# Kernel optimization log

Measured on AMD Instinct MI355X. Metric: run time of the kernel, lower is better.

Reference implementation:

```python
import jax, jax.numpy as jnp
import numpy as np

B, S, H = 32, 4096, 512


def setup_inputs() -> dict:
    key = jax.random.key(0)
    ks = jax.random.split(key, 8)
    scale = 1.0 / np.sqrt(H)
    return {
        "query": jax.random.normal(ks[0], (B, H), dtype=jnp.float32),
        "keys": jax.random.normal(ks[1], (B, S, 2 * H), dtype=jnp.float32),
        "Wa_w": jax.random.uniform(ks[2], (H, H), jnp.float32, -scale, scale),
        "Wa_b": jax.random.uniform(ks[3], (H,), jnp.float32, -scale, scale),
        "Ua_w": jax.random.uniform(ks[4], (H, 2 * H), jnp.float32, -scale, scale),
        "Ua_b": jax.random.uniform(ks[5], (H,), jnp.float32, -scale, scale),
        "Va_w": jax.random.uniform(ks[6], (1, H), jnp.float32, -scale, scale),
        "Va_b": jax.random.uniform(ks[7], (1,), jnp.float32, -scale, scale),
    }


def reference(query, keys, Wa_w, Wa_b, Ua_w, Ua_b, Va_w, Va_b):
    # query: [B,H], keys: [B,S,2H]
    q_proj = query @ Wa_w.T + Wa_b                       # [B,H]
    k_proj = jnp.einsum('bsk,hk->bsh', keys, Ua_w) + Ua_b  # [B,S,H]
    energy = jnp.tanh(q_proj[:, None, :] + k_proj)        # [B,S,H]
    scores = jnp.einsum('bsh,h->bs', energy, Va_w[0]) + Va_b[0]  # [B,S]
    attn_weights = jax.nn.softmax(scores, axis=1)         # [B,S]
    context = jnp.einsum('bs,bsk->bk', attn_weights, keys)  # [B,2H]
    return (context, attn_weights)
```

## Files before the change

kernel.cpp:

```cpp
#include <hip/hip_runtime.h>
#include <hip/hip_bf16.h>
#include <cstdint>
#include <cstddef>

#define NB 32
#define NS 4096
#define NH 512
#define NK 1024

typedef __attribute__((ext_vector_type(8))) short bf16x8;
typedef __attribute__((ext_vector_type(4))) float f32x4;

__device__ __forceinline__ short f2bf_s(float f) {
  union { float f; unsigned u; } x; x.f = f;
  unsigned r = x.u + 0x7fffu + ((x.u >> 16) & 1u);
  return (short)(r >> 16);
}

__global__ void k_ua_cvt(const float* __restrict__ ua, unsigned short* __restrict__ out) {
  int i = (blockIdx.x * 256 + threadIdx.x) * 4;
  float4 v = *(const float4*)(ua + i);
  ushort4 o;
  o.x = (unsigned short)f2bf_s(v.x);
  o.y = (unsigned short)f2bf_s(v.y);
  o.z = (unsigned short)f2bf_s(v.z);
  o.w = (unsigned short)f2bf_s(v.w);
  *(ushort4*)(out + i) = o;
}

__global__ void k_qproj(const float* __restrict__ q, const float* __restrict__ ww,
                        const float* __restrict__ wb, const float* __restrict__ ub,
                        float* __restrict__ qp) {
  int b = blockIdx.y;
  int h = blockIdx.x * 128 + threadIdx.x;
  const float* qr = q + b * NH;
  const float* wr = ww + h * NH;
  float acc = 0.f;
  for (int k = 0; k < NH; k += 4) {
    float4 a = *(const float4*)(qr + k);
    float4 c = *(const float4*)(wr + k);
    acc += a.x * c.x + a.y * c.y + a.z * c.z + a.w * c.w;
  }
  qp[b * NH + h] = acc + wb[h] + ub[h];
}

__global__ __launch_bounds__(512, 2)
void k_scores(const float* __restrict__ keys, const unsigned short* __restrict__ uabf,
              const float* __restrict__ qproj, const float* __restrict__ vaw,
              const float* __restrict__ vab, float* __restrict__ scores) {
  __shared__ uint4 lds4[2560];
  __shared__ float va_s[512];
  __shared__ float qp_s[512];

  const int b   = blockIdx.y;
  const int s0  = blockIdx.x * 128;
  const int tid = threadIdx.x;
  const int w   = tid >> 6;
  const int l   = tid & 63;
  const int col = l & 15;
  const int g   = l >> 4;

  va_s[tid] = vaw[tid];
  qp_s[tid] = qproj[b * NH + tid];

  f32x4 zero = {0.f, 0.f, 0.f, 0.f};
  f32x4 acc[32];
  #pragma unroll
  for (int i = 0; i < 32; ++i) acc[i] = zero;

  const float* arow = keys + ((size_t)b * NS + (size_t)(s0 + w * 16 + col)) * NK;

  for (int ks = 0; ks < 32; ++ks) {
    const int k0 = ks * 32;
    __syncthreads();
    #pragma unroll
    for (int i = 0; i < 4; ++i) {
      int c = (i << 9) | tid;
      int n = c >> 2, kc = c & 3;
      uint4 v = *(const uint4*)(uabf + (n << 10) + k0 + (kc << 3));
      lds4[n * 5 + kc] = v;
    }
    __syncthreads();

    const float* ap = arow + k0 + g * 8;
    float4 a0 = *(const float4*)(ap);
    float4 a1 = *(const float4*)(ap + 4);
    bf16x8 af;
    af[0] = f2bf_s(a0.x); af[1] = f2bf_s(a0.y); af[2] = f2bf_s(a0.z); af[3] = f2bf_s(a0.w);
    af[4] = f2bf_s(a1.x); af[5] = f2bf_s(a1.y); af[6] = f2bf_s(a1.z); af[7] = f2bf_s(a1.w);

    #pragma unroll
    for (int nt = 0; nt < 32; ++nt) {
      int n = (nt << 4) | col;
      bf16x8 bf = *(const bf16x8*)&lds4[n * 5 + g];
      acc[nt] = __builtin_amdgcn_mfma_f32_16x16x32_bf16(af, bf, acc[nt], 0, 0, 0);
    }
  }

  #pragma unroll
  for (int j = 0; j < 4; ++j) {
    float sc = 0.f;
    #pragma unroll
    for (int nt = 0; nt < 32; ++nt) {
      int n = (nt << 4) | col;
      sc += va_s[n] * tanhf(qp_s[n] + acc[nt][j]);
    }
    sc += __shfl_xor(sc, 1);
    sc += __shfl_xor(sc, 2);
    sc += __shfl_xor(sc, 4);
    sc += __shfl_xor(sc, 8);
    if (col == 0)
      scores[(size_t)b * NS + s0 + w * 16 + g * 4 + j] = sc + vab[0];
  }
}

__global__ void k_softmax(const float* __restrict__ scores, float* __restrict__ attn) {
  __shared__ float redm[4];
  __shared__ float reds[4];
  int b = blockIdx.x, tid = threadIdx.x;
  const float* row = scores + (size_t)b * NS;
  float v[16];
  float m = -1e30f;
  #pragma unroll
  for (int i = 0; i < 16; ++i) { v[i] = row[i * 256 + tid]; m = fmaxf(m, v[i]); }
  #pragma unroll
  for (int off = 1; off < 64; off <<= 1) m = fmaxf(m, __shfl_xor(m, off));
  if ((tid & 63) == 0) redm[tid >> 6] = m;
  __syncthreads();
  m = fmaxf(fmaxf(redm[0], redm[1]), fmaxf(redm[2], redm[3]));
  float s = 0.f;
  #pragma unroll
  for (int i = 0; i < 16; ++i) { v[i] = expf(v[i] - m); s += v[i]; }
  #pragma unroll
  for (int off = 1; off < 64; off <<= 1) s += __shfl_xor(s, off);
  if ((tid & 63) == 0) reds[tid >> 6] = s;
  __syncthreads();
  s = reds[0] + reds[1] + reds[2] + reds[3];
  float inv = 1.f / s;
  float* o = attn + (size_t)b * NS;
  #pragma unroll
  for (int i = 0; i < 16; ++i) o[i * 256 + tid] = v[i] * inv;
}

__global__ void k_ctx_partial(const float* __restrict__ keys, const float* __restrict__ attn,
                              float* __restrict__ part) {
  __shared__ float w_s[256];
  int b = blockIdx.y, seg = blockIdx.x, tid = threadIdx.x;
  int sbeg = seg * 256;
  w_s[tid] = attn[(size_t)b * NS + sbeg + tid];
  __syncthreads();
  const float* kp = keys + ((size_t)b * NS + sbeg) * NK + tid * 4;
  float ax = 0.f, ay = 0.f, az = 0.f, aw = 0.f;
  #pragma unroll 4
  for (int s = 0; s < 256; ++s) {
    float4 kv = *(const float4*)(kp + (size_t)s * NK);
    float wv = w_s[s];
    ax += wv * kv.x; ay += wv * kv.y; az += wv * kv.z; aw += wv * kv.w;
  }
  float4 o; o.x = ax; o.y = ay; o.z = az; o.w = aw;
  *(float4*)(part + ((size_t)(seg * NB + b) << 10) + tid * 4) = o;
}

__global__ void k_ctx_reduce(const float* __restrict__ part, float* __restrict__ ctx) {
  int i = blockIdx.x * 256 + threadIdx.x;
  int b = i >> 10, c = i & 1023;
  float s = 0.f;
  #pragma unroll
  for (int seg = 0; seg < 16; ++seg) s += part[((size_t)(seg * NB + b) << 10) + c];
  ctx[i] = s;
}

extern "C" void kernel_launch(void* const* d_in, const int* in_sizes, int n_in,
                              void* d_out, int out_size, void* d_ws, size_t ws_size,
                              hipStream_t stream) {
  const float* query = (const float*)d_in[0];
  const float* keys  = (const float*)d_in[1];
  const float* Wa_w  = (const float*)d_in[2];
  const float* Wa_b  = (const float*)d_in[3];
  const float* Ua_w  = (const float*)d_in[4];
  const float* Ua_b  = (const float*)d_in[5];
  const float* Va_w  = (const float*)d_in[6];
  const float* Va_b  = (const float*)d_in[7];

  float* out      = (float*)d_out;
  float* ctx_out  = out;
  float* attn_out = out + NB * NK;

  unsigned short* ua_bf = (unsigned short*)d_ws;
  float* qproj  = (float*)((char*)d_ws + (1u << 20));
  float* scores = (float*)((char*)d_ws + (1u << 20) + (1u << 16));
  float* part   = (float*)((char*)d_ws + (1u << 20) + (1u << 16) + (1u << 19));

  k_ua_cvt<<<512, 256, 0, stream>>>(Ua_w, ua_bf);
  k_qproj<<<dim3(4, NB), 128, 0, stream>>>(query, Wa_w, Wa_b, Ua_b, qproj);
  k_scores<<<dim3(NS / 128, NB), 512, 0, stream>>>(keys, ua_bf, qproj, Va_w, Va_b, scores);
  k_softmax<<<NB, 256, 0, stream>>>(scores, attn_out);
  k_ctx_partial<<<dim3(16, NB), 256, 0, stream>>>(keys, attn_out, part);
  k_ctx_reduce<<<NB * NK / 256, 256, 0, stream>>>(part, ctx_out);
}
```

Measured before the change: 472.8 us.

## Restructure scores GEMM with 32x32 MFMA, LDS-staged keys and prepacked Ua weights

Rewrites the scores kernel. Keys tiles are converted to bf16 and staged into double-buffered, XOR-swizzled LDS with prefetch of the next chunk, and Ua is prepacked into an MFMA-fragment layout read directly from global memory. Each wave now computes a 64x128 tile with 32x32x16 MFMAs instead of 16x16x32, which gives more reuse per fragment load. Also swaps tanhf for an exp-based fast tanh and adds a cross-wave LDS reduction. The cost is higher register pressure from the 8 accumulator tiles, plus a small precision change in tanh.

```diff
diff --git a/kernel.cpp b/kernel.cpp
--- a/kernel.cpp
+++ b/kernel.cpp
@@ -7,25 +7,31 @@
 #define NS 4096
 #define NH 512
 #define NK 1024
+#define KC 64
 
 typedef __attribute__((ext_vector_type(8))) short bf16x8;
 typedef __attribute__((ext_vector_type(4))) float f32x4;
-
-__device__ __forceinline__ short f2bf_s(float f) {
+typedef __attribute__((ext_vector_type(16))) float f32x16;
+
+__device__ __forceinline__ unsigned short f2bf_s(float f) {
   union { float f; unsigned u; } x; x.f = f;
   unsigned r = x.u + 0x7fffu + ((x.u >> 16) & 1u);
-  return (short)(r >> 16);
-}
-
-__global__ void k_ua_cvt(const float* __restrict__ ua, unsigned short* __restrict__ out) {
-  int i = (blockIdx.x * 256 + threadIdx.x) * 4;
-  float4 v = *(const float4*)(ua + i);
-  ushort4 o;
-  o.x = (unsigned short)f2bf_s(v.x);
-  o.y = (unsigned short)f2bf_s(v.y);
-  o.z = (unsigned short)f2bf_s(v.z);
-  o.w = (unsigned short)f2bf_s(v.w);
-  *(ushort4*)(out + i) = o;
+  return (unsigned short)(r >> 16);
+}
+
+__global__ void k_ua_pack(const float* __restrict__ ua, unsigned short* __restrict__ out) {
+  int t = blockIdx.x * 256 + threadIdx.x;
+  int l = t & 63;
+  int ct = (t >> 6) & 15;
+  int kk = t >> 10;
+  const float* src = ua + (size_t)(ct * 32 + (l & 31)) * NK + kk * 16 + (l >> 5) * 8;
+  float4 a = *(const float4*)src;
+  float4 c = *(const float4*)(src + 4);
+  ushort4 o0, o1;
+  o0.x = f2bf_s(a.x); o0.y = f2bf_s(a.y); o0.z = f2bf_s(a.z); o0.w = f2bf_s(a.w);
+  o1.x = f2bf_s(c.x); o1.y = f2bf_s(c.y); o1.z = f2bf_s(c.z); o1.w = f2bf_s(c.w);
+  ushort4* dst = (ushort4*)(out + (size_t)t * 8);
+  dst[0] = o0; dst[1] = o1;
 }
 
 __global__ void k_qproj(const float* __restrict__ q, const float* __restrict__ ww,
@@ -45,72 +51,139 @@
 }
 
 __global__ __launch_bounds__(512, 2)
-void k_scores(const float* __restrict__ keys, const unsigned short* __restrict__ uabf,
-              const float* __restrict__ qproj, const float* __restrict__ vaw,
-              const float* __restrict__ vab, float* __restrict__ scores) {
-  __shared__ uint4 lds4[2560];
-  __shared__ float va_s[512];
-  __shared__ float qp_s[512];
+void k_scores2(const float* __restrict__ keys, const unsigned short* __restrict__ uapk,
+               const float* __restrict__ qproj, const float* __restrict__ vaw,
+               const float* __restrict__ vab, float* __restrict__ scores) {
+  __shared__ alignas(16) unsigned short A_lds[2][128 * KC];
+  __shared__ float qp_s[NH];
+  __shared__ float va_s[NH];
+  __shared__ float red[128][4];
 
   const int b   = blockIdx.y;
   const int s0  = blockIdx.x * 128;
   const int tid = threadIdx.x;
   const int w   = tid >> 6;
   const int l   = tid & 63;
-  const int col = l & 15;
-  const int g   = l >> 4;
-
+  const int rg  = w >> 2;
+  const int cg  = w & 3;
+  const int l31 = l & 31;
+  const int lhi = l >> 5;
+
+  qp_s[tid] = qproj[b * NH + tid];
   va_s[tid] = vaw[tid];
-  qp_s[tid] = qproj[b * NH + tid];
-
-  f32x4 zero = {0.f, 0.f, 0.f, 0.f};
-  f32x4 acc[32];
-  #pragma unroll
-  for (int i = 0; i < 32; ++i) acc[i] = zero;
-
-  const float* arow = keys + ((size_t)b * NS + (size_t)(s0 + w * 16 + col)) * NK;
-
-  for (int ks = 0; ks < 32; ++ks) {
-    const int k0 = ks * 32;
-    __syncthreads();
+
+  const int sr  = tid & 127;
+  const int skq = tid >> 7;
+  const float* kbase = keys + ((size_t)b * NS + s0 + sr) * NK + skq * 16;
+  char* const myrow = (char*)&A_lds[0][0];
+  const int wr0 = sr * 128;
+  const int wo0 = (skq * 32) ^ ((sr & 7) << 4);
+  const int wo1 = (skq * 32 + 16) ^ ((sr & 7) << 4);
+
+  f32x16 acc[2][4];
+  #pragma unroll
+  for (int i = 0; i < 2; ++i)
     #pragma unroll
-    for (int i = 0; i < 4; ++i) {
-      int c = (i << 9) | tid;
-      int n = c >> 2, kc = c & 3;
-      uint4 v = *(const uint4*)(uabf + (n << 10) + k0 + (kc << 3));
-      lds4[n * 5 + kc] = v;
-    }
-    __syncthreads();
-
-    const float* ap = arow + k0 + g * 8;
-    float4 a0 = *(const float4*)(ap);
-    float4 a1 = *(const float4*)(ap + 4);
-    bf16x8 af;
-    af[0] = f2bf_s(a0.x); af[1] = f2bf_s(a0.y); af[2] = f2bf_s(a0.z); af[3] = f2bf_s(a0.w);
-    af[4] = f2bf_s(a1.x); af[5] = f2bf_s(a1.y); af[6] = f2bf_s(a1.z); af[7] = f2bf_s(a1.w);
-
+    for (int j = 0; j < 4; ++j)
+      #pragma unroll
+      for (int e = 0; e < 16; ++e) acc[i][j][e] = 0.f;
+
+  const int arow0 = rg * 64 + 0 * 32 + l31;
+  const int arow1 = rg * 64 + 1 * 32 + l31;
+  const int asw0 = (arow0 & 7) << 4;
+  const int asw1 = (arow1 & 7) << 4;
+
+  {
+    float4 st0 = *(const float4*)(kbase + 0);
+    float4 st1 = *(const float4*)(kbase + 4);
+    float4 st2 = *(const float4*)(kbase + 8);
+    float4 st3 = *(const float4*)(kbase + 12);
+    ushort4 p0, p1, p2, p3;
+    p0.x=f2bf_s(st0.x); p0.y=f2bf_s(st0.y); p0.z=f2bf_s(st0.z); p0.w=f2bf_s(st0.w);
+    p1.x=f2bf_s(st1.x); p1.y=f2bf_s(st1.y); p1.z=f2bf_s(st1.z); p1.w=f2bf_s(st1.w);
+    p2.x=f2bf_s(st2.x); p2.y=f2bf_s(st2.y); p2.z=f2bf_s(st2.z); p2.w=f2bf_s(st2.w);
+    p3.x=f2bf_s(st3.x); p3.y=f2bf_s(st3.y); p3.z=f2bf_s(st3.z); p3.w=f2bf_s(st3.w);
+    *(ushort4*)(myrow + wr0 + wo0)     = p0;
+    *(ushort4*)(myrow + wr0 + wo0 + 8) = p1;
+    *(ushort4*)(myrow + wr0 + wo1)     = p2;
+    *(ushort4*)(myrow + wr0 + wo1 + 8) = p3;
+  }
+  __syncthreads();
+
+  for (int c = 0; c < 16; ++c) {
+    const int buf = c & 1;
+    const char* Ab = (const char*)&A_lds[buf][0];
+    float4 nx0, nx1, nx2, nx3;
+    if (c < 15) {
+      const float* nb = kbase + (c + 1) * KC;
+      nx0 = *(const float4*)(nb + 0);
+      nx1 = *(const float4*)(nb + 4);
+      nx2 = *(const float4*)(nb + 8);
+      nx3 = *(const float4*)(nb + 12);
+    }
     #pragma unroll
-    for (int nt = 0; nt < 32; ++nt) {
-      int n = (nt << 4) | col;
-      bf16x8 bf = *(const bf16x8*)&lds4[n * 5 + g];
-      acc[nt] = __builtin_amdgcn_mfma_f32_16x16x32_bf16(af, bf, acc[nt], 0, 0, 0);
-    }
-  }
-
-  #pragma unroll
-  for (int j = 0; j < 4; ++j) {
-    float sc = 0.f;
+    for (int kk = 0; kk < 4; ++kk) {
+      const int kb = kk * 32 + lhi * 16;
+      bf16x8 af0 = *(const bf16x8*)(Ab + arow0 * 128 + (kb ^ asw0));
+      bf16x8 af1 = *(const bf16x8*)(Ab + arow1 * 128 + (kb ^ asw1));
+      const int kkg = c * 4 + kk;
+      const unsigned short* bp = uapk + (((size_t)kkg * 16 + cg * 4) * 64 + l) * 8;
+      bf16x8 bf0 = *(const bf16x8*)(bp);
+      bf16x8 bf1 = *(const bf16x8*)(bp + 64 * 8);
+      bf16x8 bf2 = *(const bf16x8*)(bp + 128 * 8);
+      bf16x8 bf3 = *(const bf16x8*)(bp + 192 * 8);
+      acc[0][0] = __builtin_amdgcn_mfma_f32_32x32x16_bf16(af0, bf0, acc[0][0], 0, 0, 0);
+      acc[1][0] = __builtin_amdgcn_mfma_f32_32x32x16_bf16(af1, bf0, acc[1][0], 0, 0, 0);
+      acc[0][1] = __builtin_amdgcn_mfma_f32_32x32x16_bf16(af0, bf1, acc[0][1], 0, 0, 0);
+      acc[1][1] = __builtin_amdgcn_mfma_f32_32x32x16_bf16(af1, bf1, acc[1][1], 0, 0, 0);
+      acc[0][2] = __builtin_amdgcn_mfma_f32_32x32x16_bf16(af0, bf2, acc[0][2], 0, 0, 0);
+      acc[1][2] = __builtin_amdgcn_mfma_f32_32x32x16_bf16(af1, bf2, acc[1][2], 0, 0, 0);
+      acc[0][3] = __builtin_amdgcn_mfma_f32_32x32x16_bf16(af0, bf3, acc[0][3], 0, 0, 0);
+      acc[1][3] = __builtin_amdgcn_mfma_f32_32x32x16_bf16(af1, bf3, acc[1][3], 0, 0, 0);
+    }
+    if (c < 15) {
+      char* Aw = (char*)&A_lds[buf ^ 1][0];
+      ushort4 p0, p1, p2, p3;
+      p0.x=f2bf_s(nx0.x); p0.y=f2bf_s(nx0.y); p0.z=f2bf_s(nx0.z); p0.w=f2bf_s(nx0.w);
+      p1.x=f2bf_s(nx1.x); p1.y=f2bf_s(nx1.y); p1.z=f2bf_s(nx1.z); p1.w=f2bf_s(nx1.w);
+      p2.x=f2bf_s(nx2.x); p2.y=f2bf_s(nx2.y); p2.z=f2bf_s(nx2.z); p2.w=f2bf_s(nx2.w);
+      p3.x=f2bf_s(nx3.x); p3.y=f2bf_s(nx3.y); p3.z=f2bf_s(nx3.z); p3.w=f2bf_s(nx3.w);
+      *(ushort4*)(Aw + wr0 + wo0)     = p0;
+      *(ushort4*)(Aw + wr0 + wo0 + 8) = p1;
+      *(ushort4*)(Aw + wr0 + wo1)     = p2;
+      *(ushort4*)(Aw + wr0 + wo1 + 8) = p3;
+      __syncthreads();
+    }
+  }
+
+  #pragma unroll
+  for (int rt = 0; rt < 2; ++rt) {
     #pragma unroll
-    for (int nt = 0; nt < 32; ++nt) {
-      int n = (nt << 4) | col;
-      sc += va_s[n] * tanhf(qp_s[n] + acc[nt][j]);
-    }
-    sc += __shfl_xor(sc, 1);
-    sc += __shfl_xor(sc, 2);
-    sc += __shfl_xor(sc, 4);
-    sc += __shfl_xor(sc, 8);
-    if (col == 0)
-      scores[(size_t)b * NS + s0 + w * 16 + g * 4 + j] = sc + vab[0];
+    for (int reg = 0; reg < 16; ++reg) {
+      float sum = 0.f;
+      #pragma unroll
+      for (int ct = 0; ct < 4; ++ct) {
+        int n = cg * 128 + ct * 32 + l31;
+        float x = qp_s[n] + acc[rt][ct][reg];
+        float e = __expf(2.f * x);
+        float th = 1.f - 2.f / (e + 1.f);
+        sum += va_s[n] * th;
+      }
+      sum += __shfl_xor(sum, 1);
+      sum += __shfl_xor(sum, 2);
+      sum += __shfl_xor(sum, 4);
+      sum += __shfl_xor(sum, 8);
+      sum += __shfl_xor(sum, 16);
+      if (l31 == 0) {
+        int rloc = (reg & 3) + 8 * (reg >> 2) + 4 * lhi;
+        red[rg * 64 + rt * 32 + rloc][cg] = sum;
+      }
+    }
+  }
+  __syncthreads();
+  if (tid < 128) {
+    float s = red[tid][0] + red[tid][1] + red[tid][2] + red[tid][3] + vab[0];
+    scores[(size_t)b * NS + s0 + tid] = s;
   }
 }
 
@@ -186,14 +259,14 @@
   float* ctx_out  = out;
   float* attn_out = out + NB * NK;
 
-  unsigned short* ua_bf = (unsigned short*)d_ws;
+  unsigned short* ua_pk = (unsigned short*)d_ws;
   float* qproj  = (float*)((char*)d_ws + (1u << 20));
   float* scores = (float*)((char*)d_ws + (1u << 20) + (1u << 16));
   float* part   = (float*)((char*)d_ws + (1u << 20) + (1u << 16) + (1u << 19));
 
-  k_ua_cvt<<<512, 256, 0, stream>>>(Ua_w, ua_bf);
+  k_ua_pack<<<256, 256, 0, stream>>>(Ua_w, ua_pk);
   k_qproj<<<dim3(4, NB), 128, 0, stream>>>(query, Wa_w, Wa_b, Ua_b, qproj);
-  k_scores<<<dim3(NS / 128, NB), 512, 0, stream>>>(keys, ua_bf, qproj, Va_w, Va_b, scores);
+  k_scores2<<<dim3(NS / 128, NB), 512, 0, stream>>>(keys, ua_pk, qproj, Va_w, Va_b, scores);
   k_softmax<<<NB, 256, 0, stream>>>(scores, attn_out);
   k_ctx_partial<<<dim3(16, NB), 256, 0, stream>>>(keys, attn_out, part);
   k_ctx_reduce<<<NB * NK / 256, 256, 0, stream>>>(part, ctx_out);
```

Measured after the change: 577.4 us. 22.1% more time.

## Retile scores GEMM into 256x256 blocks with double-buffered swizzled LDS staging

Applied to the files above, without the earlier changes.

Replaces the scores GEMM with a 256-row by 256-column tiled MFMA kernel. Keys are converted to bf16 into XOR-swizzled LDS, and the pre-packed, swizzled Ua weight is streamed in with direct global-to-LDS loads, both double-buffered across K chunks. Partial scores over two hidden-dimension halves are summed in softmax, tanh is replaced by a fast exp-based form, and the context partial segments are doubled in length. The aim is more reuse per LDS load and overlap of loads with MFMA, at the cost of larger LDS use, extra partial-score traffic and slightly lower tanh accuracy.

```diff
diff --git a/kernel.cpp b/kernel.cpp
--- a/kernel.cpp
+++ b/kernel.cpp
@@ -8,24 +8,36 @@
 #define NH 512
 #define NK 1024
 
-typedef __attribute__((ext_vector_type(8))) short bf16x8;
+typedef __attribute__((ext_vector_type(8))) short short8;
 typedef __attribute__((ext_vector_type(4))) float f32x4;
 
-__device__ __forceinline__ short f2bf_s(float f) {
+__device__ __forceinline__ unsigned short f2bf_s(float f) {
   union { float f; unsigned u; } x; x.f = f;
   unsigned r = x.u + 0x7fffu + ((x.u >> 16) & 1u);
-  return (short)(r >> 16);
-}
-
-__global__ void k_ua_cvt(const float* __restrict__ ua, unsigned short* __restrict__ out) {
-  int i = (blockIdx.x * 256 + threadIdx.x) * 4;
-  float4 v = *(const float4*)(ua + i);
-  ushort4 o;
-  o.x = (unsigned short)f2bf_s(v.x);
-  o.y = (unsigned short)f2bf_s(v.y);
-  o.z = (unsigned short)f2bf_s(v.z);
-  o.w = (unsigned short)f2bf_s(v.w);
-  *(ushort4*)(out + i) = o;
+  return (unsigned short)(r >> 16);
+}
+
+__device__ __forceinline__ void gload16(const void* g, void* l) {
+  __builtin_amdgcn_global_load_lds(
+      (const __attribute__((address_space(1))) unsigned int*)g,
+      (__attribute__((address_space(3))) unsigned int*)l, 16, 0, 0);
+}
+
+__global__ void k_ua_pack(const float* __restrict__ ua, unsigned short* __restrict__ out) {
+  int t = blockIdx.x * 256 + threadIdx.x;
+  int c = t & 2047;
+  int kc = (t >> 11) & 15;
+  int bn = t >> 15;
+  int nloc = c >> 3;
+  int k16 = (c & 7) ^ (nloc & 7);
+  const float* src = ua + (size_t)(bn * 256 + nloc) * NK + kc * 64 + k16 * 8;
+  float4 a = *(const float4*)src;
+  float4 b2 = *(const float4*)(src + 4);
+  ushort4 o0, o1;
+  o0.x = f2bf_s(a.x);  o0.y = f2bf_s(a.y);  o0.z = f2bf_s(a.z);  o0.w = f2bf_s(a.w);
+  o1.x = f2bf_s(b2.x); o1.y = f2bf_s(b2.y); o1.z = f2bf_s(b2.z); o1.w = f2bf_s(b2.w);
+  ushort4* dst = (ushort4*)(out + (size_t)t * 8);
+  dst[0] = o0; dst[1] = o1;
 }
 
 __global__ void k_qproj(const float* __restrict__ q, const float* __restrict__ ww,
@@ -45,84 +57,186 @@
 }
 
 __global__ __launch_bounds__(512, 2)
-void k_scores(const float* __restrict__ keys, const unsigned short* __restrict__ uabf,
-              const float* __restrict__ qproj, const float* __restrict__ vaw,
-              const float* __restrict__ vab, float* __restrict__ scores) {
-  __shared__ uint4 lds4[2560];
-  __shared__ float va_s[512];
-  __shared__ float qp_s[512];
-
-  const int b   = blockIdx.y;
-  const int s0  = blockIdx.x * 128;
-  const int tid = threadIdx.x;
-  const int w   = tid >> 6;
-  const int l   = tid & 63;
-  const int col = l & 15;
-  const int g   = l >> 4;
-
+void k_scores3(const float* __restrict__ keys, const unsigned short* __restrict__ uapk,
+               const float* __restrict__ qproj, const float* __restrict__ vaw,
+               float* __restrict__ scores_part) {
+  __shared__ alignas(16) unsigned short Albuf[2][256 * 64];
+  __shared__ alignas(16) unsigned short Blbuf[2][256 * 64];
+  __shared__ float qp_s[NH];
+  __shared__ float va_s[NH];
+  __shared__ float red[256][4];
+
+  const int sblk = blockIdx.x;
+  const int bn   = blockIdx.y;
+  const int b    = blockIdx.z;
+  const int tid  = threadIdx.x;
+  const int w    = tid >> 6;
+  const int l    = tid & 63;
+  const int rg   = w >> 2;
+  const int cg   = w & 3;
+  const int l15  = l & 15;
+  const int lq   = l >> 4;
+  const int asw  = (l15 & 7) << 4;
+
+  qp_s[tid] = qproj[b * NH + tid];
   va_s[tid] = vaw[tid];
-  qp_s[tid] = qproj[b * NH + tid];
-
-  f32x4 zero = {0.f, 0.f, 0.f, 0.f};
-  f32x4 acc[32];
-  #pragma unroll
-  for (int i = 0; i < 32; ++i) acc[i] = zero;
-
-  const float* arow = keys + ((size_t)b * NS + (size_t)(s0 + w * 16 + col)) * NK;
-
-  for (int ks = 0; ks < 32; ++ks) {
-    const int k0 = ks * 32;
-    __syncthreads();
+
+  const int srow = tid >> 1;
+  const int skh  = tid & 1;
+  const float* agbase = keys + ((size_t)b * NS + sblk * 256 + srow) * NK + skh * 32;
+  const int wsw = (srow & 7) << 4;
+  const int wbase = srow * 128;
+
+  const char* bgbase = (const char*)uapk + (size_t)bn * 16 * 32768 + w * 4096 + l * 16;
+
+  f32x4 acc[8][4];
+  #pragma unroll
+  for (int i = 0; i < 8; ++i)
     #pragma unroll
-    for (int i = 0; i < 4; ++i) {
-      int c = (i << 9) | tid;
-      int n = c >> 2, kc = c & 3;
-      uint4 v = *(const uint4*)(uabf + (n << 10) + k0 + (kc << 3));
-      lds4[n * 5 + kc] = v;
+    for (int j = 0; j < 4; ++j)
+      acc[i][j] = (f32x4){0.f, 0.f, 0.f, 0.f};
+
+  {
+    float4 ar0 = *(const float4*)(agbase + 0);
+    float4 ar1 = *(const float4*)(agbase + 4);
+    float4 ar2 = *(const float4*)(agbase + 8);
+    float4 ar3 = *(const float4*)(agbase + 12);
+    float4 ar4 = *(const float4*)(agbase + 16);
+    float4 ar5 = *(const float4*)(agbase + 20);
+    float4 ar6 = *(const float4*)(agbase + 24);
+    float4 ar7 = *(const float4*)(agbase + 28);
+    #pragma unroll
+    for (int j2 = 0; j2 < 4; ++j2)
+      gload16(bgbase + j2 * 1024, (char*)&Blbuf[0][0] + w * 4096 + j2 * 1024);
+    char* Aw = (char*)&Albuf[0][0];
+    short8 p0, p1, p2, p3;
+    p0[0]=f2bf_s(ar0.x); p0[1]=f2bf_s(ar0.y); p0[2]=f2bf_s(ar0.z); p0[3]=f2bf_s(ar0.w);
+    p0[4]=f2bf_s(ar1.x); p0[5]=f2bf_s(ar1.y); p0[6]=f2bf_s(ar1.z); p0[7]=f2bf_s(ar1.w);
+    p1[0]=f2bf_s(ar2.x); p1[1]=f2bf_s(ar2.y); p1[2]=f2bf_s(ar2.z); p1[3]=f2bf_s(ar2.w);
+    p1[4]=f2bf_s(ar3.x); p1[5]=f2bf_s(ar3.y); p1[6]=f2bf_s(ar3.z); p1[7]=f2bf_s(ar3.w);
+    p2[0]=f2bf_s(ar4.x); p2[1]=f2bf_s(ar4.y); p2[2]=f2bf_s(ar4.z); p2[3]=f2bf_s(ar4.w);
+    p2[4]=f2bf_s(ar5.x); p2[5]=f2bf_s(ar5.y); p2[6]=f2bf_s(ar5.z); p2[7]=f2bf_s(ar5.w);
+    p3[0]=f2bf_s(ar6.x); p3[1]=f2bf_s(ar6.y); p3[2]=f2bf_s(ar6.z); p3[3]=f2bf_s(ar6.w);
+    p3[4]=f2bf_s(ar7.x); p3[5]=f2bf_s(ar7.y); p3[6]=f2bf_s(ar7.z); p3[7]=f2bf_s(ar7.w);
+    *(short8*)(Aw + wbase + ((skh * 64 +  0) ^ wsw)) = p0;
+    *(short8*)(Aw + wbase + ((skh * 64 + 16) ^ wsw)) = p1;
+    *(short8*)(Aw + wbase + ((skh * 64 + 32) ^ wsw)) = p2;
+    *(short8*)(Aw + wbase + ((skh * 64 + 48) ^ wsw)) = p3;
+  }
+  __syncthreads();
+
+  for (int kc = 0; kc < 16; ++kc) {
+    const int cur = kc & 1;
+    const char* Ab = (const char*)&Albuf[cur][0];
+    const char* Bb = (const char*)&Blbuf[cur][0];
+
+    float4 ar0, ar1, ar2, ar3, ar4, ar5, ar6, ar7;
+    if (kc < 15) {
+      const float* ag = agbase + (kc + 1) * 64;
+      ar0 = *(const float4*)(ag + 0);
+      ar1 = *(const float4*)(ag + 4);
+      ar2 = *(const float4*)(ag + 8);
+      ar3 = *(const float4*)(ag + 12);
+      ar4 = *(const float4*)(ag + 16);
+      ar5 = *(const float4*)(ag + 20);
+      ar6 = *(const float4*)(ag + 24);
+      ar7 = *(const float4*)(ag + 28);
+      const char* bg = bgbase + (size_t)(kc + 1) * 32768;
+      #pragma unroll
+      for (int j2 = 0; j2 < 4; ++j2)
+        gload16(bg + j2 * 1024, (char*)&Blbuf[cur ^ 1][0] + w * 4096 + j2 * 1024);
+    }
+
+    #pragma unroll
+    for (int h = 0; h < 2; ++h) {
+      short8 bf[4];
+      #pragma unroll
+      for (int ct = 0; ct < 4; ++ct) {
+        int nrow = cg * 64 + ct * 16 + l15;
+        bf[ct] = *(const short8*)(Bb + nrow * 128 + ((h * 64 + lq * 16) ^ asw));
+      }
+      #pragma unroll
+      for (int rh = 0; rh < 2; ++rh) {
+        short8 af[4];
+        #pragma unroll
+        for (int r4 = 0; r4 < 4; ++r4) {
+          int arow = rg * 128 + (rh * 4 + r4) * 16 + l15;
+          af[r4] = *(const short8*)(Ab + arow * 128 + ((h * 64 + lq * 16) ^ asw));
+        }
+        __builtin_amdgcn_s_setprio(1);
+        #pragma unroll
+        for (int r4 = 0; r4 < 4; ++r4)
+          #pragma unroll
+          for (int ct = 0; ct < 4; ++ct)
+            acc[rh * 4 + r4][ct] =
+                __builtin_amdgcn_mfma_f32_16x16x32_bf16(af[r4], bf[ct], acc[rh * 4 + r4][ct], 0, 0, 0);
+        __builtin_amdgcn_s_setprio(0);
+      }
+    }
+
+    if (kc < 15) {
+      char* Aw = (char*)&Albuf[cur ^ 1][0];
+      short8 p0, p1, p2, p3;
+      p0[0]=f2bf_s(ar0.x); p0[1]=f2bf_s(ar0.y); p0[2]=f2bf_s(ar0.z); p0[3]=f2bf_s(ar0.w);
+      p0[4]=f2bf_s(ar1.x); p0[5]=f2bf_s(ar1.y); p0[6]=f2bf_s(ar1.z); p0[7]=f2bf_s(ar1.w);
+      p1[0]=f2bf_s(ar2.x); p1[1]=f2bf_s(ar2.y); p1[2]=f2bf_s(ar2.z); p1[3]=f2bf_s(ar2.w);
+      p1[4]=f2bf_s(ar3.x); p1[5]=f2bf_s(ar3.y); p1[6]=f2bf_s(ar3.z); p1[7]=f2bf_s(ar3.w);
+      p2[0]=f2bf_s(ar4.x); p2[1]=f2bf_s(ar4.y); p2[2]=f2bf_s(ar4.z); p2[3]=f2bf_s(ar4.w);
+      p2[4]=f2bf_s(ar5.x); p2[5]=f2bf_s(ar5.y); p2[6]=f2bf_s(ar5.z); p2[7]=f2bf_s(ar5.w);
+      p3[0]=f2bf_s(ar6.x); p3[1]=f2bf_s(ar6.y); p3[2]=f2bf_s(ar6.z); p3[3]=f2bf_s(ar6.w);
+      p3[4]=f2bf_s(ar7.x); p3[5]=f2bf_s(ar7.y); p3[6]=f2bf_s(ar7.z); p3[7]=f2bf_s(ar7.w);
+      *(short8*)(Aw + wbase + ((skh * 64 +  0) ^ wsw)) = p0;
+      *(short8*)(Aw + wbase + ((skh * 64 + 16) ^ wsw)) = p1;
+      *(short8*)(Aw + wbase + ((skh * 64 + 32) ^ wsw)) = p2;
+      *(short8*)(Aw + wbase + ((skh * 64 + 48) ^ wsw)) = p3;
     }
     __syncthreads();
-
-    const float* ap = arow + k0 + g * 8;
-    float4 a0 = *(const float4*)(ap);
-    float4 a1 = *(const float4*)(ap + 4);
-    bf16x8 af;
-    af[0] = f2bf_s(a0.x); af[1] = f2bf_s(a0.y); af[2] = f2bf_s(a0.z); af[3] = f2bf_s(a0.w);
-    af[4] = f2bf_s(a1.x); af[5] = f2bf_s(a1.y); af[6] = f2bf_s(a1.z); af[7] = f2bf_s(a1.w);
-
+  }
+
+  #pragma unroll
+  for (int rt = 0; rt < 8; ++rt) {
     #pragma unroll
-    for (int nt = 0; nt < 32; ++nt) {
-      int n = (nt << 4) | col;
-      bf16x8 bf = *(const bf16x8*)&lds4[n * 5 + g];
-      acc[nt] = __builtin_amdgcn_mfma_f32_16x16x32_bf16(af, bf, acc[nt], 0, 0, 0);
+    for (int reg = 0; reg < 4; ++reg) {
+      float sum = 0.f;
+      #pragma unroll
+      for (int ct = 0; ct < 4; ++ct) {
+        int gn = bn * 256 + cg * 64 + ct * 16 + l15;
+        float x = qp_s[gn] + acc[rt][ct][reg];
+        float e = __expf(2.f * x);
+        float th = 1.f - __fdividef(2.f, e + 1.f);
+        sum += va_s[gn] * th;
+      }
+      sum += __shfl_xor(sum, 1);
+      sum += __shfl_xor(sum, 2);
+      sum += __shfl_xor(sum, 4);
+      sum += __shfl_xor(sum, 8);
+      if (l15 == 0)
+        red[rg * 128 + rt * 16 + lq * 4 + reg][cg] = sum;
     }
   }
-
-  #pragma unroll
-  for (int j = 0; j < 4; ++j) {
-    float sc = 0.f;
-    #pragma unroll
-    for (int nt = 0; nt < 32; ++nt) {
-      int n = (nt << 4) | col;
-      sc += va_s[n] * tanhf(qp_s[n] + acc[nt][j]);
-    }
-    sc += __shfl_xor(sc, 1);
-    sc += __shfl_xor(sc, 2);
-    sc += __shfl_xor(sc, 4);
-    sc += __shfl_xor(sc, 8);
-    if (col == 0)
-      scores[(size_t)b * NS + s0 + w * 16 + g * 4 + j] = sc + vab[0];
-  }
-}
-
-__global__ void k_softmax(const float* __restrict__ scores, float* __restrict__ attn) {
+  __syncthreads();
+  if (tid < 256) {
+    float s = red[tid][0] + red[tid][1] + red[tid][2] + red[tid][3];
+    scores_part[((size_t)bn * NB + b) * NS + sblk * 256 + tid] = s;
+  }
+}
+
+__global__ void k_softmax(const float* __restrict__ sp, const float* __restrict__ vab,
+                          float* __restrict__ attn) {
   __shared__ float redm[4];
   __shared__ float reds[4];
   int b = blockIdx.x, tid = threadIdx.x;
-  const float* row = scores + (size_t)b * NS;
+  const float* r0 = sp + (size_t)b * NS;
+  const float* r1 = sp + (size_t)(NB + b) * NS;
+  float vb = vab[0];
   float v[16];
   float m = -1e30f;
   #pragma unroll
-  for (int i = 0; i < 16; ++i) { v[i] = row[i * 256 + tid]; m = fmaxf(m, v[i]); }
+  for (int i = 0; i < 16; ++i) {
+    int idx = i * 256 + tid;
+    v[i] = r0[idx] + r1[idx] + vb;
+    m = fmaxf(m, v[i]);
+  }
   #pragma unroll
   for (int off = 1; off < 64; off <<= 1) m = fmaxf(m, __shfl_xor(m, off));
   if ((tid & 63) == 0) redm[tid >> 6] = m;
@@ -144,15 +258,16 @@
 
 __global__ void k_ctx_partial(const float* __restrict__ keys, const float* __restrict__ attn,
                               float* __restrict__ part) {
-  __shared__ float w_s[256];
+  __shared__ float w_s[512];
   int b = blockIdx.y, seg = blockIdx.x, tid = threadIdx.x;
-  int sbeg = seg * 256;
+  int sbeg = seg * 512;
   w_s[tid] = attn[(size_t)b * NS + sbeg + tid];
+  w_s[tid + 256] = attn[(size_t)b * NS + sbeg + 256 + tid];
   __syncthreads();
   const float* kp = keys + ((size_t)b * NS + sbeg) * NK + tid * 4;
   float ax = 0.f, ay = 0.f, az = 0.f, aw = 0.f;
   #pragma unroll 4
-  for (int s = 0; s < 256; ++s) {
+  for (int s = 0; s < 512; ++s) {
     float4 kv = *(const float4*)(kp + (size_t)s * NK);
     float wv = w_s[s];
     ax += wv * kv.x; ay += wv * kv.y; az += wv * kv.z; aw += wv * kv.w;
@@ -166,7 +281,7 @@
   int b = i >> 10, c = i & 1023;
   float s = 0.f;
   #pragma unroll
-  for (int seg = 0; seg < 16; ++seg) s += part[((size_t)(seg * NB + b) << 10) + c];
+  for (int seg = 0; seg < 8; ++seg) s += part[((size_t)(seg * NB + b) << 10) + c];
   ctx[i] = s;
 }
 
@@ -186,15 +301,15 @@
   float* ctx_out  = out;
   float* attn_out = out + NB * NK;
 
-  unsigned short* ua_bf = (unsigned short*)d_ws;
+  unsigned short* ua_pk = (unsigned short*)d_ws;
   float* qproj  = (float*)((char*)d_ws + (1u << 20));
-  float* scores = (float*)((char*)d_ws + (1u << 20) + (1u << 16));
-  float* part   = (float*)((char*)d_ws + (1u << 20) + (1u << 16) + (1u << 19));
-
-  k_ua_cvt<<<512, 256, 0, stream>>>(Ua_w, ua_bf);
+  float* spart  = (float*)((char*)d_ws + (1u << 20) + (1u << 16));
+  float* part   = (float*)((char*)d_ws + (2u << 20) + (1u << 16));
+
+  k_ua_pack<<<256, 256, 0, stream>>>(Ua_w, ua_pk);
   k_qproj<<<dim3(4, NB), 128, 0, stream>>>(query, Wa_w, Wa_b, Ua_b, qproj);
-  k_scores<<<dim3(NS / 128, NB), 512, 0, stream>>>(keys, ua_bf, qproj, Va_w, Va_b, scores);
-  k_softmax<<<NB, 256, 0, stream>>>(scores, attn_out);
-  k_ctx_partial<<<dim3(16, NB), 256, 0, stream>>>(keys, attn_out, part);
+  k_scores3<<<dim3(16, 2, NB), 512, 0, stream>>>(keys, ua_pk, qproj, Va_w, spart);
+  k_softmax<<<NB, 256, 0, stream>>>(spart, Va_b, attn_out);
+  k_ctx_partial<<<dim3(8, NB), 256, 0, stream>>>(keys, attn_out, part);
   k_ctx_reduce<<<NB * NK / 256, 256, 0, stream>>>(part, ctx_out);
 }
```

Result: faster. 420.6 us (-11.1%).
